# Kernel tuning notes

Measured on AMD Instinct MI355X. Metric: run time of the kernel, lower is better.

Reference implementation:

```python
import jax, jax.numpy as jnp
import numpy as np

DIM = 3
N_FEATURES = 4
FEATURE_TABLE_SIZE = 1048576   # 2^20 (power of 2: uint32 hash math matches torch int64 exactly)
INDEX_TABLE_SIZE = 524288      # 2^19
N_LEARNABLE = 8
RESOLUTION = 128.0
N_POINTS = 500000
PRIMES = np.array([1, 2654435761, 805459861, 3674653429, 2097192037, 1434869437, 2165219737], dtype=np.uint32)

# corner mask [2^dim, dim]: True where the corner uses floor(x) on that axis
_neigs = np.arange(1 << DIM, dtype=np.int64)[:, None]
_dims = np.arange(DIM, dtype=np.int64)[None, :]
BIN_MASK = jnp.asarray((_neigs & (1 << _dims)) == 0)


def setup_inputs() -> dict:
    key = jax.random.key(0)
    k1, k2, k3 = jax.random.split(key, 3)
    x = jax.random.uniform(k1, (N_POINTS, DIM), dtype=jnp.float32)
    feature_table = jax.random.uniform(k2, (FEATURE_TABLE_SIZE, N_FEATURES), dtype=jnp.float32,
                                       minval=-1e-4, maxval=1e-4)
    index_table = jax.random.normal(k3, (INDEX_TABLE_SIZE, N_LEARNABLE), dtype=jnp.float32)
    return {"x": x, "feature_table": feature_table, "index_table": index_table}


def _fast_hash(inds):
    # inds: [N, 2^dim, dim] int32 (nonnegative). tiny-cuda-nn fast hash in uint32
    u = inds.astype(jnp.uint32) * jnp.asarray(PRIMES[:DIM])
    h = u[..., 0]
    for i in range(1, DIM):
        h = h ^ u[..., i]
    return h % jnp.uint32(INDEX_TABLE_SIZE)  # uint32 [N, 2^dim]


def reference(x, feature_table, index_table):
    softmax_t = 1.0
    xs = x * RESOLUTION                                   # [N, dim]
    xi = xs.astype(jnp.int32)                             # trunc == floor for x >= 0
    xf = xs - jax.lax.stop_gradient(xi.astype(xs.dtype))  # fractional part, grads flow through xs
    xi = xi[:, None, :]                                   # [N, 1, dim]
    xf = xf[:, None, :]
    inds = jnp.where(BIN_MASK, xi, xi + 1)                # [N, 2^dim, dim]
    ws = jnp.where(BIN_MASK, 1.0 - xf, xf)
    w = jnp.prod(ws, axis=-1, keepdims=True)              # trilinear weights [N, 2^dim, 1]

    hash_ids = _fast_hash(inds)                           # uint32 [N, 2^dim]
    feature_weights = index_table[hash_ids.astype(jnp.int32)]  # [N, 2^dim, L]

    # second (index->feature-table) hash; power-of-2 modulus makes uint32 exact
    ar = jnp.arange(N_LEARNABLE, dtype=jnp.uint32)[None, None, :]
    a = (ar * jnp.uint32(PRIMES[1])) ^ (hash_ids[:, :, None] * jnp.uint32(PRIMES[2]))
    a = (a % jnp.uint32(FEATURE_TABLE_SIZE)).astype(jnp.int32)   # [N, 2^dim, L]

    features = feature_table[a]                                  # [N, 2^dim, L, F]
    fw = jax.nn.softmax(feature_weights * softmax_t, axis=-1)    # [N, 2^dim, L]
    features = jnp.sum(features * fw[..., None], axis=-2)        # [N, 2^dim, F]
    out = jnp.sum(features * w, axis=-2)                         # [N, F]
    return out
```

## Files before the change

### kernel.cpp

```cpp
#include <hip/hip_runtime.h>

#define NPOINTS 500000
#define RESOLUTION 128.0f
#define IDX_SIZE 524288u
#define IDX_MASK 0x7FFFFu
#define FEAT_MASK 0xFFFFFu
#define P1 2654435761u
#define P2 805459861u

typedef float    f4v __attribute__((ext_vector_type(4)));
typedef unsigned u2v __attribute__((ext_vector_type(2)));

constexpr unsigned mulinv32(unsigned a) {
    unsigned x = 1u;
    for (int i = 0; i < 6; ++i) x *= 2u - a * x;
    return x;
}
constexpr unsigned P2INV = mulinv32(P2);
static_assert(((P2INV * P2) & FEAT_MASK) == 1u, "bad inverse");

__device__ inline unsigned bf16pack(float a, float b) {
    unsigned ua = __float_as_uint(a); ua = (ua + 0x7FFFu + ((ua >> 16) & 1u)) >> 16;
    unsigned ub = __float_as_uint(b); ub = (ub + 0x7FFFu + ((ub >> 16) & 1u)) >> 16;
    return ua | (ub << 16);
}

__global__ __launch_bounds__(256) void build_F_y(
    const f4v* __restrict__ ftp,
    const float* __restrict__ index_table,
    u2v* __restrict__ F)
{
    unsigned y = blockIdx.x * blockDim.x + threadIdx.x;
    unsigned h = (y * P2INV) & FEAT_MASK;
    if (h >= IDX_SIZE) return;

    const f4v* p = (const f4v*)(index_table + (size_t)h * 8u);
    f4v iw0 = p[0];
    f4v iw1 = p[1];

    f4v fv[8];
#pragma unroll
    for (unsigned j = 0; j < 8; ++j) {
        unsigned cj = (j * P1) & FEAT_MASK;
        fv[j] = ftp[y ^ cj];
    }

    float e[8] = { iw0.x, iw0.y, iw0.z, iw0.w, iw1.x, iw1.y, iw1.z, iw1.w };
    float mx = fmaxf(fmaxf(fmaxf(e[0], e[1]), fmaxf(e[2], e[3])),
                     fmaxf(fmaxf(e[4], e[5]), fmaxf(e[6], e[7])));
    float s = 0.f;
#pragma unroll
    for (int j = 0; j < 8; ++j) { e[j] = __expf(e[j] - mx); s += e[j]; }

    float ax = 0.f, ay = 0.f, az = 0.f, aw = 0.f;
#pragma unroll
    for (int j = 0; j < 8; ++j) {
        ax = fmaf(fv[j].x, e[j], ax);
        ay = fmaf(fv[j].y, e[j], ay);
        az = fmaf(fv[j].z, e[j], az);
        aw = fmaf(fv[j].w, e[j], aw);
    }
    float inv = 1.0f / s;
    ax *= inv; ay *= inv; az *= inv; aw *= inv;

    u2v packed;
    packed.x = bf16pack(ax, ay);
    packed.y = bf16pack(az, aw);
    F[h] = packed;
}

__global__ __launch_bounds__(256) void interp2(
    const float* __restrict__ x,
    const u2v* __restrict__ F,
    float4* __restrict__ out)
{
    int t = blockIdx.x * blockDim.x + threadIdx.x;
    int p0 = t << 1;
    if (p0 >= NPOINTS) return;

    unsigned hs[16];
    float    ws[16];
#pragma unroll
    for (int r = 0; r < 2; ++r) {
        int p = p0 + r;
        float xs0 = x[p * 3 + 0] * RESOLUTION;
        float xs1 = x[p * 3 + 1] * RESOLUTION;
        float xs2 = x[p * 3 + 2] * RESOLUTION;
        int i0 = (int)xs0, i1 = (int)xs1, i2 = (int)xs2;
        float f0 = xs0 - (float)i0, f1 = xs1 - (float)i1, f2 = xs2 - (float)i2;
        float g0 = 1.0f - f0, g1 = 1.0f - f1, g2 = 1.0f - f2;
        unsigned u0 = (unsigned)i0;
        unsigned m1a = (unsigned)i1 * P1, m1b = ((unsigned)i1 + 1u) * P1;
        unsigned m2a = (unsigned)i2 * P2, m2b = ((unsigned)i2 + 1u) * P2;
#pragma unroll
        for (int c = 0; c < 8; ++c) {
            unsigned b0 = c & 1, b1 = (c >> 1) & 1, b2 = (c >> 2) & 1;
            hs[r * 8 + c] = ((u0 + b0) ^ (b1 ? m1b : m1a) ^ (b2 ? m2b : m2a)) & IDX_MASK;
            ws[r * 8 + c] = (b0 ? f0 : g0) * (b1 ? f1 : g1) * (b2 ? f2 : g2);
        }
    }

    u2v fv[16];
#pragma unroll
    for (int k = 0; k < 16; ++k) fv[k] = F[hs[k]];

#pragma unroll
    for (int r = 0; r < 2; ++r) {
        float ax = 0.f, ay = 0.f, az = 0.f, aw = 0.f;
#pragma unroll
        for (int c = 0; c < 8; ++c) {
            int k = r * 8 + c;
            float fx = __uint_as_float(fv[k].x << 16);
            float fy = __uint_as_float(fv[k].x & 0xFFFF0000u);
            float fz = __uint_as_float(fv[k].y << 16);
            float fw = __uint_as_float(fv[k].y & 0xFFFF0000u);
            ax = fmaf(fx, ws[k], ax);
            ay = fmaf(fy, ws[k], ay);
            az = fmaf(fz, ws[k], az);
            aw = fmaf(fw, ws[k], aw);
        }
        out[p0 + r] = make_float4(ax, ay, az, aw);
    }
}

__global__ __launch_bounds__(256) void hashgrid_fwd(
    const float* __restrict__ x,
    const float* __restrict__ feature_table,
    const float* __restrict__ index_table,
    float* __restrict__ out)
{
    int tid = blockIdx.x * blockDim.x + threadIdx.x;
    int p = tid >> 3;
    int corner = tid & 7;
    if (p >= NPOINTS) return;

    float xs0 = x[p * 3 + 0] * RESOLUTION;
    float xs1 = x[p * 3 + 1] * RESOLUTION;
    float xs2 = x[p * 3 + 2] * RESOLUTION;
    int i0 = (int)xs0, i1 = (int)xs1, i2 = (int)xs2;
    float f0 = xs0 - (float)i0, f1 = xs1 - (float)i1, f2 = xs2 - (float)i2;

    unsigned b0 = corner & 1u, b1 = (corner >> 1) & 1u, b2 = (corner >> 2) & 1u;
    unsigned ind0 = (unsigned)i0 + b0;
    unsigned ind1 = (unsigned)i1 + b1;
    unsigned ind2 = (unsigned)i2 + b2;
    float w0 = b0 ? f0 : 1.0f - f0;
    float w1 = b1 ? f1 : 1.0f - f1;
    float w2 = b2 ? f2 : 1.0f - f2;
    float w = w0 * w1 * w2;

    unsigned h = (ind0 ^ ind1 * P1 ^ ind2 * P2) & IDX_MASK;

    const float4* itp = (const float4*)(index_table + (size_t)h * 8u);
    float4 iw0 = itp[0];
    float4 iw1 = itp[1];
    float e0 = iw0.x, e1 = iw0.y, e2 = iw0.z, e3 = iw0.w;
    float e4 = iw1.x, e5 = iw1.y, e6 = iw1.z, e7 = iw1.w;

    float mx = fmaxf(fmaxf(fmaxf(e0, e1), fmaxf(e2, e3)),
                     fmaxf(fmaxf(e4, e5), fmaxf(e6, e7)));
    e0 = __expf(e0 - mx); e1 = __expf(e1 - mx);
    e2 = __expf(e2 - mx); e3 = __expf(e3 - mx);
    e4 = __expf(e4 - mx); e5 = __expf(e5 - mx);
    e6 = __expf(e6 - mx); e7 = __expf(e7 - mx);
    float s = ((e0 + e1) + (e2 + e3)) + ((e4 + e5) + (e6 + e7));

    unsigned hp2 = h * P2;
    const float4* ftp = (const float4*)feature_table;
    float ax = 0.f, ay = 0.f, az = 0.f, aw = 0.f;
    float ej[8] = {e0, e1, e2, e3, e4, e5, e6, e7};
#pragma unroll
    for (unsigned j = 0; j < 8; ++j) {
        unsigned a = ((j * P1) ^ hp2) & FEAT_MASK;
        float4 ft = ftp[a];
        ax = fmaf(ft.x, ej[j], ax);
        ay = fmaf(ft.y, ej[j], ay);
        az = fmaf(ft.z, ej[j], az);
        aw = fmaf(ft.w, ej[j], aw);
    }

    float scale = w / s;
    ax *= scale; ay *= scale; az *= scale; aw *= scale;

#pragma unroll
    for (int m = 1; m < 8; m <<= 1) {
        ax += __shfl_xor(ax, m);
        ay += __shfl_xor(ay, m);
        az += __shfl_xor(az, m);
        aw += __shfl_xor(aw, m);
    }
    if (corner == 0) {
        ((float4*)out)[p] = make_float4(ax, ay, az, aw);
    }
}

extern "C" void kernel_launch(void* const* d_in, const int* in_sizes, int n_in,
                              void* d_out, int out_size, void* d_ws, size_t ws_size,
                              hipStream_t stream) {
    const float* x  = (const float*)d_in[0];
    const float* ft = (const float*)d_in[1];
    const float* it = (const float*)d_in[2];

    const size_t F_BYTES = (size_t)IDX_SIZE * 8u;

    if (ws_size >= F_BYTES) {
        u2v* F = (u2v*)d_ws;
        hipLaunchKernelGGL(build_F_y, dim3((1u << 20) / 256), dim3(256), 0, stream,
                           (const f4v*)ft, it, F);
        const int lanes2 = NPOINTS / 2;
        hipLaunchKernelGGL(interp2, dim3((lanes2 + 255) / 256), dim3(256), 0, stream,
                           x, F, (float4*)d_out);
    } else {
        const int total = NPOINTS * 8;
        hipLaunchKernelGGL(hashgrid_fwd, dim3((total + 255) / 256), dim3(256), 0, stream,
                           x, ft, it, (float*)d_out);
    }
}
```

Baseline: 57.72 us.

## Pre-pack feature table to bf16 before building the index-feature table

```diff
diff --git a/kernel.cpp b/kernel.cpp
--- a/kernel.cpp
+++ b/kernel.cpp
@@ -10,6 +10,7 @@
 
 typedef float    f4v __attribute__((ext_vector_type(4)));
 typedef unsigned u2v __attribute__((ext_vector_type(2)));
+typedef unsigned u4v __attribute__((ext_vector_type(4)));
 
 constexpr unsigned mulinv32(unsigned a) {
     unsigned x = 1u;
@@ -23,6 +24,62 @@
     unsigned ua = __float_as_uint(a); ua = (ua + 0x7FFFu + ((ua >> 16) & 1u)) >> 16;
     unsigned ub = __float_as_uint(b); ub = (ub + 0x7FFFu + ((ub >> 16) & 1u)) >> 16;
     return ua | (ub << 16);
+}
+__device__ inline float bf16lo(unsigned u) { return __uint_as_float(u << 16); }
+__device__ inline float bf16hi(unsigned u) { return __uint_as_float(u & 0xFFFF0000u); }
+
+__global__ __launch_bounds__(256) void pack_ft16(
+    const f4v* __restrict__ ftp,
+    u2v* __restrict__ ft16)
+{
+    unsigned i = blockIdx.x * blockDim.x + threadIdx.x;
+    f4v v = ftp[i];
+    u2v o;
+    o.x = bf16pack(v.x, v.y);
+    o.y = bf16pack(v.z, v.w);
+    ft16[i] = o;
+}
+
+__global__ __launch_bounds__(256) void build_F_y16(
+    const u2v* __restrict__ ft16,
+    const float* __restrict__ index_table,
+    u2v* __restrict__ F)
+{
+    unsigned y = blockIdx.x * blockDim.x + threadIdx.x;
+    unsigned h = (y * P2INV) & FEAT_MASK;
+    if (h >= IDX_SIZE) return;
+
+    const f4v* p = (const f4v*)(index_table + (size_t)h * 8u);
+    f4v iw0 = p[0];
+    f4v iw1 = p[1];
+
+    u2v fv[8];
+#pragma unroll
+    for (unsigned j = 0; j < 8; ++j) {
+        unsigned cj = (j * P1) & FEAT_MASK;
+        fv[j] = ft16[y ^ cj];
+    }
+
+    float e[8] = { iw0.x, iw0.y, iw0.z, iw0.w, iw1.x, iw1.y, iw1.z, iw1.w };
+    float mx = fmaxf(fmaxf(fmaxf(e[0], e[1]), fmaxf(e[2], e[3])),
+                     fmaxf(fmaxf(e[4], e[5]), fmaxf(e[6], e[7])));
+    float s = 0.f;
+#pragma unroll
+    for (int j = 0; j < 8; ++j) { e[j] = __expf(e[j] - mx); s += e[j]; }
+
+    float ax = 0.f, ay = 0.f, az = 0.f, aw = 0.f;
+#pragma unroll
+    for (int j = 0; j < 8; ++j) {
+        ax = fmaf(bf16lo(fv[j].x), e[j], ax);
+        ay = fmaf(bf16hi(fv[j].x), e[j], ay);
+        az = fmaf(bf16lo(fv[j].y), e[j], az);
+        aw = fmaf(bf16hi(fv[j].y), e[j], aw);
+    }
+    float inv = 1.0f / s;
+    u2v packed;
+    packed.x = bf16pack(ax * inv, ay * inv);
+    packed.y = bf16pack(az * inv, aw * inv);
+    F[h] = packed;
 }
 
 __global__ __launch_bounds__(256) void build_F_y(
@@ -61,18 +118,16 @@
         aw = fmaf(fv[j].w, e[j], aw);
     }
     float inv = 1.0f / s;
-    ax *= inv; ay *= inv; az *= inv; aw *= inv;
-
     u2v packed;
-    packed.x = bf16pack(ax, ay);
-    packed.y = bf16pack(az, aw);
+    packed.x = bf16pack(ax * inv, ay * inv);
+    packed.y = bf16pack(az * inv, aw * inv);
     F[h] = packed;
 }
 
 __global__ __launch_bounds__(256) void interp2(
     const float* __restrict__ x,
     const u2v* __restrict__ F,
-    float4* __restrict__ out)
+    f4v* __restrict__ out)
 {
     int t = blockIdx.x * blockDim.x + threadIdx.x;
     int p0 = t << 1;
@@ -102,7 +157,7 @@
 
     u2v fv[16];
 #pragma unroll
-    for (int k = 0; k < 16; ++k) fv[k] = F[hs[k]];
+    for (int k = 0; k < 16; ++k) fv[k] = __builtin_nontemporal_load(F + hs[k]);
 
 #pragma unroll
     for (int r = 0; r < 2; ++r) {
@@ -110,16 +165,13 @@
 #pragma unroll
         for (int c = 0; c < 8; ++c) {
             int k = r * 8 + c;
-            float fx = __uint_as_float(fv[k].x << 16);
-            float fy = __uint_as_float(fv[k].x & 0xFFFF0000u);
-            float fz = __uint_as_float(fv[k].y << 16);
-            float fw = __uint_as_float(fv[k].y & 0xFFFF0000u);
-            ax = fmaf(fx, ws[k], ax);
-            ay = fmaf(fy, ws[k], ay);
-            az = fmaf(fz, ws[k], az);
-            aw = fmaf(fw, ws[k], aw);
+            ax = fmaf(bf16lo(fv[k].x), ws[k], ax);
+            ay = fmaf(bf16hi(fv[k].x), ws[k], ay);
+            az = fmaf(bf16lo(fv[k].y), ws[k], az);
+            aw = fmaf(bf16hi(fv[k].y), ws[k], aw);
         }
-        out[p0 + r] = make_float4(ax, ay, az, aw);
+        f4v o = { ax, ay, az, aw };
+        out[p0 + r] = o;
     }
 }
 
@@ -141,15 +193,13 @@
     float f0 = xs0 - (float)i0, f1 = xs1 - (float)i1, f2 = xs2 - (float)i2;
 
     unsigned b0 = corner & 1u, b1 = (corner >> 1) & 1u, b2 = (corner >> 2) & 1u;
-    unsigned ind0 = (unsigned)i0 + b0;
-    unsigned ind1 = (unsigned)i1 + b1;
-    unsigned ind2 = (unsigned)i2 + b2;
     float w0 = b0 ? f0 : 1.0f - f0;
     float w1 = b1 ? f1 : 1.0f - f1;
     float w2 = b2 ? f2 : 1.0f - f2;
     float w = w0 * w1 * w2;
 
-    unsigned h = (ind0 ^ ind1 * P1 ^ ind2 * P2) & IDX_MASK;
+    unsigned h = (((unsigned)i0 + b0) ^ (((unsigned)i1 + b1) * P1)
+                  ^ (((unsigned)i2 + b2) * P2)) & IDX_MASK;
 
     const float4* itp = (const float4*)(index_table + (size_t)h * 8u);
     float4 iw0 = itp[0];
@@ -201,15 +251,26 @@
     const float* ft = (const float*)d_in[1];
     const float* it = (const float*)d_in[2];
 
-    const size_t F_BYTES = (size_t)IDX_SIZE * 8u;
-
-    if (ws_size >= F_BYTES) {
+    const size_t F_BYTES    = (size_t)IDX_SIZE * 8u;
+    const size_t FT16_BYTES = (size_t)(1u << 20) * 8u;
+
+    if (ws_size >= F_BYTES + FT16_BYTES) {
+        u2v* F    = (u2v*)d_ws;
+        u2v* ft16 = (u2v*)((char*)d_ws + F_BYTES);
+        hipLaunchKernelGGL(pack_ft16, dim3((1u << 20) / 256), dim3(256), 0, stream,
+                           (const f4v*)ft, ft16);
+        hipLaunchKernelGGL(build_F_y16, dim3((1u << 20) / 256), dim3(256), 0, stream,
+                           ft16, it, F);
+        const int lanes2 = NPOINTS / 2;
+        hipLaunchKernelGGL(interp2, dim3((lanes2 + 255) / 256), dim3(256), 0, stream,
+                           x, F, (f4v*)d_out);
+    } else if (ws_size >= F_BYTES) {
         u2v* F = (u2v*)d_ws;
         hipLaunchKernelGGL(build_F_y, dim3((1u << 20) / 256), dim3(256), 0, stream,
                            (const f4v*)ft, it, F);
         const int lanes2 = NPOINTS / 2;
         hipLaunchKernelGGL(interp2, dim3((lanes2 + 255) / 256), dim3(256), 0, stream,
-                           x, F, (float4*)d_out);
+                           x, F, (f4v*)d_out);
     } else {
         const int total = NPOINTS * 8;
         hipLaunchKernelGGL(hashgrid_fwd, dim3((total + 255) / 256), dim3(256), 0, stream,
```

After: 81.26 us. 1.41x slower.
